# Kernel optimization log

Hardware: AMD Instinct MI355X
Metric: run time of the kernel (lower is better)

Reference implementation:

```python
import jax, jax.numpy as jnp
import numpy as np

N, NNODES, CIN, COUT = 64, 512, 32, 64


def setup_inputs() -> dict:
    key = jax.random.key(0)
    k1, k2, k3, k4, k5 = jax.random.split(key, 5)
    A = jax.random.normal(k1, (N, NNODES, NNODES), dtype=jnp.float32)
    X = jax.random.normal(k2, (N, NNODES, CIN), dtype=jnp.float32)
    A_coeffs = jax.random.normal(k3, (5 + 2 * CIN,), dtype=jnp.float32)
    x_num = 4 + 2 * CIN
    scale = np.sqrt(2.0) / (COUT + x_num)
    X_coeffs_1 = jax.random.normal(k4, (COUT, x_num), dtype=jnp.float32) * scale
    X_coeffs_2 = jax.random.normal(k5, (COUT, x_num), dtype=jnp.float32) * scale
    return {"A": A, "X": X, "A_coeffs": A_coeffs,
            "X_coeffs_1": X_coeffs_1, "X_coeffs_2": X_coeffs_2}


def _forward(A, X, A_coeffs, W1, W2):
    n = A.shape[-1]
    C = X.shape[-1]
    Xt = jnp.swapaxes(X, -1, -2)                      # N,C,n
    diag = jnp.diagonal(A, axis1=-2, axis2=-1)        # N,n
    mean_diag = diag.mean(-1)                         # N
    mean_cols = A.mean(-1)                            # N,n
    mean_all = mean_cols.mean(-1)                     # N
    mean_X = Xt.mean(-1)                              # N,C

    c = A_coeffs
    w6 = c[5:5 + C]                                   # coeffs for a6 (X_i + X_j)
    w7 = c[5 + C:5 + 2 * C]                           # coeffs for a7 (mean_X)
    # Fold the 'd,ndij->nij' contraction over the 7 basis tensors into
    # scalar/row/col broadcast terms (identical math, no N x (5+2C) x n x n tensor).
    s = jnp.einsum('c,nci->ni', w6, Xt)               # N,n
    const = c[1] * mean_all + c[2] * mean_diag + jnp.einsum('c,nc->n', w7, mean_X)
    vec = c[3] * mean_cols + c[4] * diag + s          # N,n
    A_t = c[0] * A + const[:, None, None] + vec[:, :, None] + vec[:, None, :]

    # X basis out_x: N x (4+2C) x n, order [x1, x2, x3, x4, x5, x6]
    ones_n = jnp.ones((1, 1, n), A.dtype)
    out_x = jnp.concatenate([
        Xt,                                           # x1: N,C,n
        mean_X[:, :, None] * ones_n,                  # x2: N,C,n
        mean_cols[:, None, :],                        # x3: N,1,n
        diag[:, None, :],                             # x4: N,1,n
        mean_diag[:, None, None] * ones_n,            # x5: N,1,n
        mean_all[:, None, None] * ones_n,             # x6: N,1,n
    ], axis=1)
    X1 = jnp.einsum('bd,ndi->nbi', W1, out_x)         # N,B,n
    X2 = jnp.einsum('bd,ndi->nbi', W2, out_x)         # N,B,n
    out = jnp.einsum('nij,nbj->nbi', A_t, X1) / n + X2  # N,B,n
    return jnp.swapaxes(out, -1, -2)                  # N,n,B


def reference(A, X, A_coeffs, X_coeffs_1, X_coeffs_2):
    return _forward(A, X, A_coeffs, X_coeffs_1, X_coeffs_2)
```

## Files before the change

### kernel.cpp

```cpp
#include <hip/hip_runtime.h>
#include <hip/hip_bf16.h>

#define NB 64
#define NN 512
#define CI 32
#define CO 64
#define XN 68

typedef __attribute__((ext_vector_type(8))) short bf16x8;
typedef __attribute__((ext_vector_type(4))) float f32x4;

__device__ inline short f2bf(float f) {
  union { __hip_bfloat16 h; unsigned short u; } cv;
  cv.h = __float2bfloat16(f);
  return (short)cv.u;
}

__device__ inline bf16x8 cvt8(float4 a, float4 b) {
  bf16x8 r;
  r[0] = f2bf(a.x); r[1] = f2bf(a.y); r[2] = f2bf(a.z); r[3] = f2bf(a.w);
  r[4] = f2bf(b.x); r[5] = f2bf(b.y); r[6] = f2bf(b.z); r[7] = f2bf(b.w);
  return r;
}

__global__ __launch_bounds__(256) void k1x(
    const float* __restrict__ A, const float* __restrict__ X,
    const float* __restrict__ cf, const float* __restrict__ W1,
    float* __restrict__ mc, float* __restrict__ dg, float* __restrict__ vec,
    float* __restrict__ pA, float* __restrict__ pD,
    float* __restrict__ pmX, float* __restrict__ ptC, float* __restrict__ pS,
    unsigned short* __restrict__ Ybf, unsigned short* __restrict__ Abf) {
  int b = blockIdx.x, ch = blockIdx.y;
  int t = threadIdx.x, w = t >> 6, lane = t & 63;
  int r0 = ch * 16;
  int kb = r0 >> 5, jbase = r0 & 16;
  const float* Ab = A + (size_t)b * NN * NN;
  __shared__ float sXc[16][33];
  __shared__ float scf[69];
  __shared__ float sMc[16], sDg[16], sVec[16], wsum[4];

  if (t < 69) scf[t] = cf[t];
  {
    int j = t >> 4, c = (t & 15) * 2;
    float2 xv = *(const float2*)(X + ((size_t)b * NN + r0 + j) * CI + c);
    sXc[j][c] = xv.x; sXc[j][c + 1] = xv.y;
  }
  float4 v0[4], v1[4];
#pragma unroll
  for (int m = 0; m < 4; ++m) {
    const float* rp = Ab + (size_t)(r0 + w * 4 + m) * NN;
    v0[m] = *(const float4*)(rp + lane * 4);
    v1[m] = *(const float4*)(rp + 256 + lane * 4);
  }
  float accR = 0.f;
#pragma unroll
  for (int m = 0; m < 4; ++m) {
    float s = (v0[m].x + v0[m].y) + (v0[m].z + v0[m].w) +
              (v1[m].x + v1[m].y) + (v1[m].z + v1[m].w);
#pragma unroll
    for (int off = 1; off < 64; off <<= 1) s += __shfl_xor(s, off, 64);
    if (lane == 0) {
      float m_ = s * (1.0f / NN);
      mc[b * NN + r0 + w * 4 + m] = m_;
      sMc[w * 4 + m] = m_;
    }
    accR += s;
  }
  if (lane == 0) wsum[w] = accR;
  if (t < 16) {
    float d = Ab[(size_t)(r0 + t) * NN + r0 + t];
    dg[b * NN + r0 + t] = d;
    sDg[t] = d;
  }

  {
    int ic5 = ch >> 2;
    int lrb = (ch & 3) * 16 + w * 4;
    size_t bb = ((size_t)(b * 8 + ic5)) * 8 * 4096;
    int c5a = lane >> 4;
    int Ka = (lane & 15) >> 1;
    int sub = (lane & 1) << 2;
#pragma unroll
    for (int m = 0; m < 4; ++m) {
      int lr = lrb + m;
      int sl = ((Ka ^ (lr & 7)) << 3) + sub;
      union { unsigned short u[4]; uint2 v; } p0, p1;
      p0.u[0] = (unsigned short)f2bf(v0[m].x); p0.u[1] = (unsigned short)f2bf(v0[m].y);
      p0.u[2] = (unsigned short)f2bf(v0[m].z); p0.u[3] = (unsigned short)f2bf(v0[m].w);
      p1.u[0] = (unsigned short)f2bf(v1[m].x); p1.u[1] = (unsigned short)f2bf(v1[m].y);
      p1.u[2] = (unsigned short)f2bf(v1[m].z); p1.u[3] = (unsigned short)f2bf(v1[m].w);
      *(uint2*)(Abf + bb + (size_t)c5a * 4096 + lr * 64 + sl) = p0.v;
      *(uint2*)(Abf + bb + (size_t)(4 + c5a) * 4096 + lr * 64 + sl) = p1.v;
    }
  }
  __syncthreads();

  float c0n = scf[0] * (1.0f / NN);

  if (t < 16) {
    float u = 0.f;
#pragma unroll
    for (int c = 0; c < CI; ++c) u += scf[5 + c] * sXc[t][c];
    float vj = scf[3] * sMc[t] + scf[4] * sDg[t] + u;
    vec[b * NN + r0 + t] = vj;
    sVec[t] = vj;
  } else if (t == 16) {
    pA[b * 32 + ch] = wsum[0] + wsum[1] + wsum[2] + wsum[3];
    float sd = 0.f;
#pragma unroll
    for (int k = 0; k < 16; ++k) sd += sDg[k];
    pD[b * 32 + ch] = sd;
  }

  {
    int ra = lane & 15, kg = lane >> 4, g = lane >> 4;
    const float* wp = W1 + (w * 16 + ra) * XN + kg * 8;
    bf16x8 wf = cvt8(*(const float4*)wp, *(const float4*)(wp + 4));
    const float* xp = &sXc[ra][kg * 8];
    bf16x8 xf = cvt8(*(const float4*)xp, *(const float4*)(xp + 4));
    f32x4 zero = {0.f, 0.f, 0.f, 0.f};
    f32x4 d = __builtin_amdgcn_mfma_f32_16x16x32_bf16(xf, wf, zero, 0, 0, 0);
    union { unsigned short u[4]; uint2 v; } pk;
#pragma unroll
    for (int r = 0; r < 4; ++r) pk.u[r] = (unsigned short)f2bf(d[r] * c0n);
    int o = w * 16 + ra;
    *(uint2*)(Ybf + (((size_t)b * 16 + kb) * 80 + o) * 32 + jbase + g * 4) = pk.v;
  }
  if (t < 16) {
    Ybf[(((size_t)b * 16 + kb) * 80 + 64) * 32 + jbase + t] =
        (unsigned short)f2bf(sMc[t] * c0n);
  } else if (t < 32) {
    Ybf[(((size_t)b * 16 + kb) * 80 + 65) * 32 + jbase + (t - 16)] =
        (unsigned short)f2bf(sDg[t - 16] * c0n);
  } else if (t < 32 + 224) {
    int u2 = t - 32;
    int row = 66 + (u2 >> 4), col = jbase + (u2 & 15);
    Ybf[(((size_t)b * 16 + kb) * 80 + row) * 32 + col] = 0;
  }
  __syncthreads();

  if (t < 32) {
    float s1 = 0.f, s2 = 0.f;
#pragma unroll
    for (int r = 0; r < 16; ++r) {
      float xv = sXc[r][t];
      s1 += xv;
      s2 += sVec[r] * xv;
    }
    pmX[((size_t)b * 32 + ch) * 32 + t] = s1;
    ptC[((size_t)b * 32 + ch) * 32 + t] = s2;
  } else if (t < 35) {
    float s = 0.f;
    if (t == 32) { for (int r = 0; r < 16; ++r) s += sVec[r]; }
    if (t == 33) { for (int r = 0; r < 16; ++r) s += sVec[r] * sMc[r]; }
    if (t == 34) { for (int r = 0; r < 16; ++r) s += sVec[r] * sDg[r]; }
    pS[((size_t)b * 32 + ch) * 3 + (t - 32)] = s;
  }
}

__global__ __launch_bounds__(256) void kW(
    const float* __restrict__ cf, const float* __restrict__ W1,
    const float* __restrict__ W2, const float* __restrict__ pA,
    const float* __restrict__ pD, const float* __restrict__ pmX,
    const float* __restrict__ ptC, const float* __restrict__ pS,
    float* __restrict__ colv, float* __restrict__ sconst) {
  int gb = blockIdx.x, t = threadIdx.x;
  int bb0 = gb * 4;
  __shared__ float sW1[64][69], sW2[64][69];
  __shared__ float mXs[4][33], tCs[4][33];
  __shared__ float scal[4][6];
  __shared__ float scf[69];
  if (t < 69) scf[t] = cf[t];
  for (int idx = t; idx < 64 * XN; idx += 256) {
    int r = idx / XN, c = idx - r * XN;
    sW1[r][c] = W1[idx];
    sW2[r][c] = W2[idx];
  }
  if (t < 128) {
    int bb = t >> 5, c = t & 31, b = bb0 + bb;
    float s1 = 0.f, s2 = 0.f;
#pragma unroll
    for (int k = 0; k < 32; ++k) {
      s1 += pmX[((size_t)b * 32 + k) * 32 + c];
      s2 += ptC[((size_t)b * 32 + k) * 32 + c];
    }
    mXs[bb][c] = s1 * (1.0f / NN);
    tCs[bb][c] = s2;
  } else if (t < 132) {
    int bb = t - 128, b = bb0 + bb;
    float sA = 0.f, sD = 0.f;
#pragma unroll
    for (int k = 0; k < 32; ++k) { sA += pA[b * 32 + k]; sD += pD[b * 32 + k]; }
    scal[bb][0] = sD * (1.0f / NN);
    scal[bb][1] = sA * (1.0f / ((float)NN * (float)NN));
  } else if (t < 136) {
    int bb = t - 132, b = bb0 + bb;
    float s1 = 0.f, s2 = 0.f, s3 = 0.f;
#pragma unroll
    for (int k = 0; k < 32; ++k) {
      s1 += pS[((size_t)b * 32 + k) * 3 + 0];
      s2 += pS[((size_t)b * 32 + k) * 3 + 1];
      s3 += pS[((size_t)b * 32 + k) * 3 + 2];
    }
    scal[bb][2] = s1; scal[bb][3] = s2; scal[bb][4] = s3;
  }
  __syncthreads();
  if (t < 4) {
    float s7 = 0.f;
#pragma unroll
    for (int c = 0; c < CI; ++c) s7 += scf[5 + CI + c] * mXs[t][c];
    sconst[bb0 + t] = scf[1] * scal[t][1] + scf[2] * scal[t][0] + s7;
  }
  {
    int bb = t >> 6, o = t & 63, b = bb0 + bb;
    float w1mX = 0.f, a1 = 0.f, a2 = 0.f, wt = 0.f;
#pragma unroll
    for (int c = 0; c < CI; ++c) {
      float m = mXs[bb][c];
      w1mX += sW1[o][c] * m;
      a1 += sW1[o][CI + c] * m;
      a2 += sW2[o][CI + c] * m;
      wt += sW1[o][c] * tCs[bb][c];
    }
    float smd = scal[bb][0], sma = scal[bb][1];
    a1 += sW1[o][66] * smd + sW1[o][67] * sma;
    a2 += sW2[o][66] * smd + sW2[o][67] * sma;
    float we0 = sW1[o][64], we1 = sW1[o][65];
    float S1n = w1mX + a1 + we0 * sma + we1 * smd;
    float SVn = (wt + a1 * scal[bb][2] + we0 * scal[bb][3] + we1 * scal[bb][4]) * (1.0f / NN);
    float4 cva = make_float4(S1n, a2 + SVn, sW2[o][64] + scf[0] * a1, sW2[o][65]);
    float4 cvb = make_float4(we0, we1, 0.f, 0.f);
    *(float4*)&colv[((size_t)b * CO + o) * 8] = cva;
    *(float4*)&colv[((size_t)b * CO + o) * 8 + 4] = cvb;
  }
}

__global__ __launch_bounds__(512, 2) void k5_mfma(
    const unsigned short* __restrict__ Abf, const unsigned short* __restrict__ Ybf,
    const float* __restrict__ X, const float* __restrict__ W2,
    const float* __restrict__ vec, const float* __restrict__ mc,
    const float* __restrict__ dg, const float* __restrict__ colv,
    const float* __restrict__ sconst, float* __restrict__ out) {
  int ic = blockIdx.x, b = blockIdx.y;
  int t = threadIdx.x, w = t >> 6, lane = t & 63;
  int rg = w >> 1, oc = w & 1;
  int ra = lane & 15, kg = lane >> 4, g = lane >> 4;
  int i0 = ic * 64;
  int wr0 = rg * 16;
  __shared__ unsigned short sA[2][4096];
  __shared__ unsigned short sB[2][160 * 40];
  __shared__ float sGm[64], sGd[64];

  const unsigned short* Asrc = Abf + ((size_t)(b * 8 + ic)) * 8 * 4096;
  const unsigned short* Yb = Ybf + (size_t)b * 16 * 80 * 32;

  int b1_row = t >> 2, b1_sub = t & 3;
  int b2_row = 128 + (t >> 2), b2_sub = t & 3;
  bool hasb2 = (t < 128);

  {
    uint4 av = *(const uint4*)(Asrc + t * 8);
    *(uint4*)&sA[0][t * 8] = av;
    uint4 v1 = *(const uint4*)(Yb + b1_row * 32 + b1_sub * 8);
    *(uint4*)&sB[0][b1_row * 40 + b1_sub * 8] = v1;
    if (hasb2) {
      uint4 v2 = *(const uint4*)(Yb + b2_row * 32 + b2_sub * 8);
      *(uint4*)&sB[0][b2_row * 40 + b2_sub * 8] = v2;
    }
  }
  uint4 rCa = *(const uint4*)(Asrc + 4096 + t * 8);
  uint4 rCb1 = *(const uint4*)(Yb + 160 * 32 + b1_row * 32 + b1_sub * 8);
  uint4 rCb2;
  if (hasb2) rCb2 = *(const uint4*)(Yb + 160 * 32 + b2_row * 32 + b2_sub * 8);
  __syncthreads();

  f32x4 acc[2] = {{0.f, 0.f, 0.f, 0.f}, {0.f, 0.f, 0.f, 0.f}};
  f32x4 acc4 = {0.f, 0.f, 0.f, 0.f};
  int arow = wr0 + ra;
  int abase = arow * 64;
  int aswz = arow & 7;

  for (int c = 0; c < 8; ++c) {
    int cur = c & 1;
    uint4 rNa, rNb1, rNb2;
    if (c < 6) {
      rNa = *(const uint4*)(Asrc + (size_t)(c + 2) * 4096 + t * 8);
      const unsigned short* nsrc = Yb + (size_t)(c + 2) * 160 * 32;
      rNb1 = *(const uint4*)(nsrc + b1_row * 32 + b1_sub * 8);
      if (hasb2) rNb2 = *(const uint4*)(nsrc + b2_row * 32 + b2_sub * 8);
    }
    __builtin_amdgcn_sched_barrier(0);
#pragma unroll
    for (int kbl = 0; kbl < 2; ++kbl) {
      bf16x8 af = *(const bf16x8*)&sA[cur][abase + (((kbl * 4 + kg) ^ aswz) << 3)];
#pragma unroll
      for (int to = 0; to < 2; ++to) {
        int grow = kbl * 80 + oc * 32 + to * 16 + ra;
        bf16x8 bf = *(const bf16x8*)&sB[cur][grow * 40 + kg * 8];
        acc[to] = __builtin_amdgcn_mfma_f32_16x16x32_bf16(af, bf, acc[to], 0, 0, 0);
      }
      if (oc == 0) {
        bf16x8 bf4 = *(const bf16x8*)&sB[cur][(kbl * 80 + 64 + ra) * 40 + kg * 8];
        acc4 = __builtin_amdgcn_mfma_f32_16x16x32_bf16(af, bf4, acc4, 0, 0, 0);
      }
    }
    if (c < 7) {
      *(uint4*)&sA[cur ^ 1][t * 8] = rCa;
      *(uint4*)&sB[cur ^ 1][b1_row * 40 + b1_sub * 8] = rCb1;
      if (hasb2) *(uint4*)&sB[cur ^ 1][b2_row * 40 + b2_sub * 8] = rCb2;
      rCa = rNa; rCb1 = rNb1;
      if (hasb2) rCb2 = rNb2;
    }
    __syncthreads();
  }

  {
    const float* xp = X + (size_t)(b * NN + i0 + wr0 + ra) * CI + kg * 8;
    bf16x8 xf = cvt8(*(const float4*)xp, *(const float4*)(xp + 4));
#pragma unroll
    for (int to = 0; to < 2; ++to) {
      const float* wp = W2 + (size_t)(oc * 32 + to * 16 + ra) * XN + kg * 8;
      bf16x8 wf = cvt8(*(const float4*)wp, *(const float4*)(wp + 4));
      acc[to] = __builtin_amdgcn_mfma_f32_16x16x32_bf16(xf, wf, acc[to], 0, 0, 0);
    }
  }

  if (oc == 0 && ra < 2) {
#pragma unroll
    for (int r = 0; r < 4; ++r) {
      if (ra == 0) sGm[wr0 + g * 4 + r] = acc4[r];
      else         sGd[wr0 + g * 4 + r] = acc4[r];
    }
  }
  __syncthreads();

  float4 v4 = *(const float4*)&vec[b * NN + i0 + wr0 + g * 4];
  float4 m4 = *(const float4*)&mc[b * NN + i0 + wr0 + g * 4];
  float4 d4 = *(const float4*)&dg[b * NN + i0 + wr0 + g * 4];
  float sc = sconst[b];
  float vp[4] = {v4.x + sc, v4.y + sc, v4.z + sc, v4.w + sc};
  float mr[4] = {m4.x, m4.y, m4.z, m4.w};
  float dr[4] = {d4.x, d4.y, d4.z, d4.w};
  float Gm[4], Gd[4];
#pragma unroll
  for (int r = 0; r < 4; ++r) {
    int row = wr0 + g * 4 + r;
    Gm[r] = sGm[row];
    Gd[r] = sGd[row];
  }

#pragma unroll
  for (int to = 0; to < 2; ++to) {
    int o = oc * 32 + to * 16 + ra;
    float4 cva = *(const float4*)&colv[((size_t)b * CO + o) * 8];
    float4 cvb = *(const float4*)&colv[((size_t)b * CO + o) * 8 + 4];
#pragma unroll
    for (int r = 0; r < 4; ++r) {
      float val = acc[to][r] + vp[r] * cva.x + cva.y + mr[r] * cva.z +
                  dr[r] * cva.w + Gm[r] * cvb.x + Gd[r] * cvb.y;
      out[((size_t)(b * NN + i0 + wr0 + g * 4 + r)) * CO + o] = val;
    }
  }
}

extern "C" void kernel_launch(void* const* d_in, const int* in_sizes, int n_in,
                              void* d_out, int out_size, void* d_ws, size_t ws_size,
                              hipStream_t stream) {
  const float* A = (const float*)d_in[0];
  const float* X = (const float*)d_in[1];
  const float* cf = (const float*)d_in[2];
  const float* W1 = (const float*)d_in[3];
  const float* W2 = (const float*)d_in[4];
  float* out = (float*)d_out;

  float* p = (float*)d_ws;
  float* mc = p;      p += NB * NN;
  float* dg = p;      p += NB * NN;
  float* vec = p;     p += NB * NN;
  float* pA = p;      p += NB * 32;
  float* pD = p;      p += NB * 32;
  float* pmX = p;     p += NB * 32 * 32;
  float* ptC = p;     p += NB * 32 * 32;
  float* pS = p;      p += NB * 32 * 3;
  float* colv = p;    p += NB * CO * 8;
  float* sconst = p;  p += NB;
  unsigned short* Ybf = (unsigned short*)p;
  unsigned short* Abf = Ybf + (size_t)NB * 16 * 80 * 32;

  k1x<<<dim3(NB, 32), 256, 0, stream>>>(A, X, cf, W1, mc, dg, vec,
                                        pA, pD, pmX, ptC, pS, Ybf, Abf);
  kW<<<16, 256, 0, stream>>>(cf, W1, W2, pA, pD, pmX, ptC, pS, colv, sconst);
  k5_mfma<<<dim3(8, NB), 512, 0, stream>>>(Abf, Ybf, X, W2, vec, mc, dg,
                                           colv, sconst, out);
}
```

Baseline: 45.87 us.

## Fuse pipeline into one cooperative kernel with a grid-wide sync

Replaces the three-kernel pipeline with a single cooperative kernel over 256 blocks. Each block keeps its 128 A rows in LDS as bf16, computes row statistics and its part of the Y operand, publishes partial sums, then grid-syncs and runs the MFMA matmul and epilogue directly from LDS. This removes the bf16 A round trip through global memory and two kernel launch boundaries. In exchange it adds a grid barrier, atomic relaxed loads and stores for the shared buffers, and a large LDS footprint that must still allow all blocks to be co-resident; if the cooperative launch fails, the old three-kernel path runs instead.

```diff
diff --git a/kernel.cpp b/kernel.cpp
--- a/kernel.cpp
+++ b/kernel.cpp
@@ -1,5 +1,6 @@
 #include <hip/hip_runtime.h>
 #include <hip/hip_bf16.h>
+#include <hip/hip_cooperative_groups.h>
 
 #define NB 64
 #define NN 512
@@ -15,12 +16,296 @@
   cv.h = __float2bfloat16(f);
   return (short)cv.u;
 }
-
+__device__ inline float bf2f(unsigned short u) {
+  union { unsigned int i; float f; } c;
+  c.i = ((unsigned int)u) << 16;
+  return c.f;
+}
 __device__ inline bf16x8 cvt8(float4 a, float4 b) {
   bf16x8 r;
   r[0] = f2bf(a.x); r[1] = f2bf(a.y); r[2] = f2bf(a.z); r[3] = f2bf(a.w);
   r[4] = f2bf(b.x); r[5] = f2bf(b.y); r[6] = f2bf(b.z); r[7] = f2bf(b.w);
   return r;
+}
+__device__ inline void astore8(unsigned short* p, unsigned long long v) {
+  __hip_atomic_store((unsigned long long*)p, v, __ATOMIC_RELAXED,
+                     __HIP_MEMORY_SCOPE_AGENT);
+}
+__device__ inline void astoref(float* p, float v) {
+  __hip_atomic_store(p, v, __ATOMIC_RELAXED, __HIP_MEMORY_SCOPE_AGENT);
+}
+__device__ inline float aloadf(const float* p) {
+  return __hip_atomic_load((float*)p, __ATOMIC_RELAXED, __HIP_MEMORY_SCOPE_AGENT);
+}
+__device__ inline bf16x8 aload16(const unsigned short* p) {
+  union { unsigned long long q[2]; bf16x8 v; } u;
+  u.q[0] = __hip_atomic_load((unsigned long long*)p, __ATOMIC_RELAXED,
+                             __HIP_MEMORY_SCOPE_AGENT);
+  u.q[1] = __hip_atomic_load((unsigned long long*)p + 1, __ATOMIC_RELAXED,
+                             __HIP_MEMORY_SCOPE_AGENT);
+  return u.v;
+}
+
+__global__ __launch_bounds__(512, 2) void kmain(
+    const float* __restrict__ A, const float* __restrict__ X,
+    const float* __restrict__ cf, const float* __restrict__ W1,
+    const float* __restrict__ W2,
+    float* __restrict__ pA, float* __restrict__ pD, float* __restrict__ pS,
+    float* __restrict__ pmX, float* __restrict__ ptC,
+    unsigned short* __restrict__ Ybf, float* __restrict__ out) {
+  int ic = blockIdx.x, b = blockIdx.y;
+  int t = threadIdx.x, w = t >> 6, lane = t & 63;
+  int i0 = ic * 128;
+
+  __shared__ unsigned short sA[8 * 128 * 64];
+  __shared__ unsigned short sXfh[128][32];
+  __shared__ float sMc[128], sDg[128], sVec[128], sRs[128];
+  __shared__ float sColv[64 * 8];
+  __shared__ float scf[72];
+  __shared__ float sStat[8];
+  __shared__ float sMXs[32], sTCs[32];
+
+  if (t < 69) scf[t] = cf[t];
+
+  int r = t >> 2, s = t & 3;
+  int row_g = i0 + r;
+  const float* Arow = A + ((size_t)(b * NN) + row_g) * NN;
+  {
+    const float* xp = X + ((size_t)(b * NN) + row_g) * CI + s * 8;
+    float4 x0 = *(const float4*)xp, x1 = *(const float4*)(xp + 4);
+    *(bf16x8*)&sXfh[r][s * 8] = cvt8(x0, x1);
+  }
+  float rowsum = 0.f;
+  int s_d = row_g >> 7, g_d = (row_g & 127) >> 4, e_d = row_g & 15;
+#pragma unroll
+  for (int g8 = 0; g8 < 8; ++g8) {
+    int col = s * 128 + g8 * 16;
+    float4 a0 = *(const float4*)(Arow + col);
+    float4 a1 = *(const float4*)(Arow + col + 4);
+    float4 a2 = *(const float4*)(Arow + col + 8);
+    float4 a3 = *(const float4*)(Arow + col + 12);
+    rowsum += (a0.x + a0.y) + (a0.z + a0.w) + (a1.x + a1.y) + (a1.z + a1.w) +
+              (a2.x + a2.y) + (a2.z + a2.w) + (a3.x + a3.y) + (a3.z + a3.w);
+    if (s == s_d && g8 == g_d) {
+      int q = e_d >> 2, e = e_d & 3;
+      float4 pick = (q == 0) ? a0 : (q == 1) ? a1 : (q == 2) ? a2 : a3;
+      sDg[r] = (&pick.x)[e];
+    }
+    int c64 = col >> 6, c0 = col & 63;
+    int sl0 = c0 >> 3;
+    int base = (c64 * 128 + r) * 64;
+    *(bf16x8*)&sA[base + ((sl0 ^ (r & 7)) << 3)] = cvt8(a0, a1);
+    *(bf16x8*)&sA[base + (((sl0 + 1) ^ (r & 7)) << 3)] = cvt8(a2, a3);
+  }
+  rowsum += __shfl_xor(rowsum, 1, 64);
+  rowsum += __shfl_xor(rowsum, 2, 64);
+  if (s == 0) {
+    sRs[r] = rowsum;
+    sMc[r] = rowsum * (1.0f / NN);
+  }
+  __syncthreads();
+
+  float c0n = scf[0] * (1.0f / NN);
+
+  if (t < 128) {
+    float u = 0.f;
+#pragma unroll
+    for (int c = 0; c < CI; ++c) u += scf[5 + c] * bf2f(sXfh[t][c]);
+    sVec[t] = scf[3] * sMc[t] + scf[4] * sDg[t] + u;
+  }
+  __syncthreads();
+
+  {
+    int ra = lane & 15, kg = lane >> 4, g = lane >> 4;
+    int j0 = w * 16;
+    bf16x8 xf = *(const bf16x8*)&sXfh[j0 + ra][kg * 8];
+#pragma unroll
+    for (int to = 0; to < 4; ++to) {
+      const float* wp = W1 + (to * 16 + ra) * XN + kg * 8;
+      bf16x8 wf = cvt8(*(const float4*)wp, *(const float4*)(wp + 4));
+      f32x4 zero = {0.f, 0.f, 0.f, 0.f};
+      f32x4 d = __builtin_amdgcn_mfma_f32_16x16x32_bf16(xf, wf, zero, 0, 0, 0);
+      int o = to * 16 + ra;
+      int jg = i0 + j0 + g * 4;
+      int kb = jg >> 5, colj = jg & 31;
+      union { unsigned short u4[4]; unsigned long long q; } pk;
+#pragma unroll
+      for (int rr = 0; rr < 4; ++rr) pk.u4[rr] = (unsigned short)f2bf(d[rr] * c0n);
+      astore8(&Ybf[(((size_t)b * 16 + kb) * 80 + o) * 32 + colj], pk.q);
+    }
+  }
+  if (t < 64) {
+    int isdg = t >> 5, p = t & 31;
+    int jg = i0 + p * 4;
+    int kb = jg >> 5, colj = jg & 31;
+    union { unsigned short u4[4]; unsigned long long q; } pk;
+#pragma unroll
+    for (int k = 0; k < 4; ++k) {
+      float v = (isdg ? sDg[p * 4 + k] : sMc[p * 4 + k]) * c0n;
+      pk.u4[k] = (unsigned short)f2bf(v);
+    }
+    astore8(&Ybf[(((size_t)b * 16 + kb) * 80 + 64 + isdg) * 32 + colj], pk.q);
+  }
+  if (t < 448) {
+    int kb_i = t / 112, rem = t % 112;
+    int rr = 66 + rem / 8, c8 = (rem % 8) * 4;
+    astore8(&Ybf[(((size_t)b * 16 + 4 * ic + kb_i) * 80 + rr) * 32 + c8], 0ULL);
+  }
+  if (t < 32) {
+    float s1 = 0.f, s2 = 0.f;
+    for (int rr = 0; rr < 128; ++rr) {
+      float xvv = bf2f(sXfh[rr][t]);
+      s1 += xvv;
+      s2 += sVec[rr] * xvv;
+    }
+    astoref(&pmX[((size_t)b * 4 + ic) * 32 + t], s1);
+    astoref(&ptC[((size_t)b * 4 + ic) * 32 + t], s2);
+  } else if (t == 32) {
+    float sa = 0.f, sd = 0.f;
+    for (int rr = 0; rr < 128; ++rr) { sa += sRs[rr]; sd += sDg[rr]; }
+    astoref(&pA[b * 4 + ic], sa);
+    astoref(&pD[b * 4 + ic], sd);
+  } else if (t < 36) {
+    int k = t - 33;
+    float ss = 0.f;
+    if (k == 0) for (int rr = 0; rr < 128; ++rr) ss += sVec[rr];
+    if (k == 1) for (int rr = 0; rr < 128; ++rr) ss += sVec[rr] * sMc[rr];
+    if (k == 2) for (int rr = 0; rr < 128; ++rr) ss += sVec[rr] * sDg[rr];
+    astoref(&pS[((size_t)b * 4 + ic) * 3 + k], ss);
+  }
+
+  __threadfence();
+  cooperative_groups::this_grid().sync();
+  __threadfence();
+
+  if (t < 32) {
+    float s1 = 0.f, s2 = 0.f;
+#pragma unroll
+    for (int k = 0; k < 4; ++k) {
+      s1 += aloadf(&pmX[((size_t)b * 4 + k) * 32 + t]);
+      s2 += aloadf(&ptC[((size_t)b * 4 + k) * 32 + t]);
+    }
+    sMXs[t] = s1 * (1.0f / NN);
+    sTCs[t] = s2;
+  } else if (t == 32) {
+    float sa = 0.f, sd = 0.f;
+#pragma unroll
+    for (int k = 0; k < 4; ++k) {
+      sa += aloadf(&pA[b * 4 + k]);
+      sd += aloadf(&pD[b * 4 + k]);
+    }
+    sStat[1] = sa * (1.0f / ((float)NN * (float)NN));
+    sStat[0] = sd * (1.0f / NN);
+  } else if (t == 33) {
+    float s1 = 0.f, s2 = 0.f, s3 = 0.f;
+#pragma unroll
+    for (int k = 0; k < 4; ++k) {
+      s1 += aloadf(&pS[((size_t)b * 4 + k) * 3 + 0]);
+      s2 += aloadf(&pS[((size_t)b * 4 + k) * 3 + 1]);
+      s3 += aloadf(&pS[((size_t)b * 4 + k) * 3 + 2]);
+    }
+    sStat[3] = s1; sStat[4] = s2; sStat[5] = s3;
+  }
+  __syncthreads();
+  if (t == 0) {
+    float s7 = 0.f;
+#pragma unroll
+    for (int c = 0; c < CI; ++c) s7 += scf[5 + CI + c] * sMXs[c];
+    sStat[2] = scf[1] * sStat[1] + scf[2] * sStat[0] + s7;
+  }
+  if (t < CO) {
+    int o = t;
+    const float* w1 = W1 + o * XN;
+    const float* w2 = W2 + o * XN;
+    float w1mX = 0.f, a1 = 0.f, a2 = 0.f, wt = 0.f;
+#pragma unroll
+    for (int c = 0; c < CI; ++c) {
+      float m = sMXs[c];
+      w1mX += w1[c] * m;
+      a1 += w1[CI + c] * m;
+      a2 += w2[CI + c] * m;
+      wt += w1[c] * sTCs[c];
+    }
+    float smd = sStat[0], sma = sStat[1];
+    a1 += w1[66] * smd + w1[67] * sma;
+    a2 += w2[66] * smd + w2[67] * sma;
+    float we0 = w1[64], we1 = w1[65];
+    float S1n = w1mX + a1 + we0 * sma + we1 * smd;
+    float SVn = (wt + a1 * sStat[3] + we0 * sStat[4] + we1 * sStat[5]) * (1.0f / NN);
+    sColv[o * 8 + 0] = S1n;
+    sColv[o * 8 + 1] = a2 + SVn;
+    sColv[o * 8 + 2] = w2[64] + scf[0] * a1;
+    sColv[o * 8 + 3] = w2[65];
+    sColv[o * 8 + 4] = we0;
+    sColv[o * 8 + 5] = we1;
+  }
+  __syncthreads();
+
+  {
+    int ra = lane & 15, kg = lane >> 4, g = lane >> 4;
+    int wr0 = w * 16;
+    int rr_ = wr0 + ra;
+    const unsigned short* Yb = Ybf + (size_t)b * 16 * 2560;
+
+    f32x4 acc[4] = {{0.f, 0.f, 0.f, 0.f}, {0.f, 0.f, 0.f, 0.f},
+                    {0.f, 0.f, 0.f, 0.f}, {0.f, 0.f, 0.f, 0.f}};
+    f32x4 acc4 = {0.f, 0.f, 0.f, 0.f};
+
+#pragma unroll
+    for (int jj = 0; jj < 16; ++jj) {
+      int c64 = jj >> 1, kbl = jj & 1;
+      bf16x8 af = *(const bf16x8*)&sA[(c64 * 128 + rr_) * 64 +
+                                      (((kbl * 4 + kg) ^ (rr_ & 7)) << 3)];
+      const unsigned short* Bb = Yb + (size_t)jj * 2560;
+#pragma unroll
+      for (int to = 0; to < 4; ++to) {
+        bf16x8 bf = aload16(&Bb[(to * 16 + ra) * 32 + kg * 8]);
+        acc[to] = __builtin_amdgcn_mfma_f32_16x16x32_bf16(af, bf, acc[to], 0, 0, 0);
+      }
+      bf16x8 b4 = aload16(&Bb[(64 + ra) * 32 + kg * 8]);
+      acc4 = __builtin_amdgcn_mfma_f32_16x16x32_bf16(af, b4, acc4, 0, 0, 0);
+    }
+
+    {
+      bf16x8 xf2 = *(const bf16x8*)&sXfh[rr_][kg * 8];
+#pragma unroll
+      for (int to = 0; to < 4; ++to) {
+        const float* wp = W2 + (size_t)(to * 16 + ra) * XN + kg * 8;
+        bf16x8 wf = cvt8(*(const float4*)wp, *(const float4*)(wp + 4));
+        acc[to] = __builtin_amdgcn_mfma_f32_16x16x32_bf16(xf2, wf, acc[to], 0, 0, 0);
+      }
+    }
+
+    float Gm[4], Gd[4];
+#pragma unroll
+    for (int rr = 0; rr < 4; ++rr) {
+      Gm[rr] = __shfl(acc4[rr], lane & 48, 64);
+      Gd[rr] = __shfl(acc4[rr], (lane & 48) | 1, 64);
+    }
+
+    float sc = sStat[2];
+    float vp[4], mr[4], dr[4];
+#pragma unroll
+    for (int rr = 0; rr < 4; ++rr) {
+      int row = wr0 + g * 4 + rr;
+      vp[rr] = sVec[row] + sc;
+      mr[rr] = sMc[row];
+      dr[rr] = sDg[row];
+    }
+
+#pragma unroll
+    for (int to = 0; to < 4; ++to) {
+      int o = to * 16 + ra;
+      float4 cva = *(const float4*)&sColv[o * 8];
+      float vb0 = sColv[o * 8 + 4], vb1 = sColv[o * 8 + 5];
+#pragma unroll
+      for (int rr = 0; rr < 4; ++rr) {
+        float val = acc[to][rr] + vp[rr] * cva.x + cva.y + mr[rr] * cva.z +
+                    dr[rr] * cva.w + Gm[rr] * vb0 + Gd[rr] * vb1;
+        out[((size_t)(b * NN + i0 + wr0 + g * 4 + rr)) * CO + o] = val;
+      }
+    }
+  }
 }
 
 __global__ __launch_bounds__(256) void k1x(
@@ -72,7 +357,6 @@
     dg[b * NN + r0 + t] = d;
     sDg[t] = d;
   }
-
   {
     int ic5 = ch >> 2;
     int lrb = (ch & 3) * 16 + w * 4;
@@ -111,7 +395,6 @@
     for (int k = 0; k < 16; ++k) sd += sDg[k];
     pD[b * 32 + ch] = sd;
   }
-
   {
     int ra = lane & 15, kg = lane >> 4, g = lane >> 4;
     const float* wp = W1 + (w * 16 + ra) * XN + kg * 8;
@@ -373,6 +656,24 @@
   const float* W2 = (const float*)d_in[4];
   float* out = (float*)d_out;
 
+  {
+    float* p = (float*)d_ws;
+    float* cpA = p;   p += NB * 4;
+    float* cpD = p;   p += NB * 4;
+    float* cpS = p;   p += NB * 4 * 3;
+    float* cpmX = p;  p += NB * 4 * 32;
+    float* cptC = p;  p += NB * 4 * 32;
+    unsigned short* cYbf = (unsigned short*)p;
+
+    void* kargs[] = {(void*)&A, (void*)&X, (void*)&cf, (void*)&W1, (void*)&W2,
+                     (void*)&cpA, (void*)&cpD, (void*)&cpS, (void*)&cpmX,
+                     (void*)&cptC, (void*)&cYbf, (void*)&out};
+    hipError_t err = hipLaunchCooperativeKernel((void*)kmain, dim3(4, NB),
+                                                dim3(512), kargs, 0, stream);
+    if (err == hipSuccess) return;
+    (void)hipGetLastError();
+  }
+
   float* p = (float*)d_ws;
   float* mc = p;      p += NB * NN;
   float* dg = p;      p += NB * NN;
```

New measurement: 164.3 us. +258.2%, slower.
